# Kernel optimization log

Hardware: AMD Instinct MI355X
Metric: run time of the kernel (lower is better)

The kernel has to match this reference:

```python
import jax, jax.numpy as jnp
import numpy as np

SEQ, BATCH, D, N = 256, 4, 512, 32768
TEMP = 0.5


def setup_inputs() -> dict:
    key = jax.random.key(0)
    ks = jax.random.split(key, 16)
    d = D
    # xavier_uniform with gain 1/sqrt(2) for square [d,d]: limit = gain*sqrt(6/(d+d))
    lim_t = (1.0 / np.sqrt(2.0)) * np.sqrt(6.0 / (d + d))
    lim_g1 = np.sqrt(6.0 / (2 * d + d))  # default kaiming-ish scale approximated by xavier
    lim_g2 = np.sqrt(6.0 / (d + 1))
    inp = {
        "q": jax.random.normal(ks[0], (SEQ, BATCH, D), dtype=jnp.float32),
        "prev_layer_output": jax.random.normal(ks[1], (SEQ, BATCH, D), dtype=jnp.float32),
        "Wq": jax.random.uniform(ks[2], (D, D), jnp.float32, -lim_t, lim_t),
        "bq": jnp.zeros((D,), jnp.float32),
        "Wk": jax.random.uniform(ks[3], (D, D), jnp.float32, -lim_t, lim_t),
        "bk": jnp.zeros((D,), jnp.float32),
        "Wv": jax.random.uniform(ks[4], (D, D), jnp.float32, -lim_t, lim_t),
        "bv": jnp.zeros((D,), jnp.float32),
        "Wg1": jax.random.uniform(ks[5], (D, 2 * D), jnp.float32, -lim_g1, lim_g1),
        "bg1": jnp.zeros((D,), jnp.float32),
        "Wg2": jax.random.uniform(ks[6], (1, D), jnp.float32, -lim_g2, lim_g2),
        "bg2": jnp.zeros((1,), jnp.float32),
        "dstore_k": jax.random.normal(ks[7], (N, D), dtype=jnp.float32),
        "dstore_v": jax.random.normal(ks[8], (N, D), dtype=jnp.float32),
    }
    return inp


def reference(q, prev_layer_output, Wq, bq, Wk, bk, Wv, bv, Wg1, bg1, Wg2, bg2, dstore_k, dstore_v):
    # [S,B,D] -> [B,S,D]
    qb = jnp.transpose(q, (1, 0, 2))
    prevb = jnp.transpose(prev_layer_output, (1, 0, 2))
    # enable_tune projections
    _q = qb @ Wq.T + bq                      # [B,S,D]
    _k = dstore_k @ Wk.T + bk                # [N,D]
    _v = dstore_v @ Wv.T + bv                # [N,D]
    _q = _q * (D ** -0.5)
    # attention over datastore, temperature-scaled softmax
    logits = jnp.einsum("bsd,nd->bsn", _q, _k) / TEMP  # [B,S,N]
    w = jax.nn.softmax(logits, axis=-1)
    attn = jnp.einsum("bsn,nd->bsd", w, _v)            # [B,S,D]
    # gated residual fusion
    cat = jnp.concatenate([attn, prevb], axis=-1)      # [B,S,2D]
    h = jax.nn.relu(cat @ Wg1.T + bg1)                 # [B,S,D]
    sigma = jax.nn.sigmoid(h @ Wg2.T + bg2)            # [B,S,1]
    res = attn * sigma + prevb * (1.0 - sigma)
    return jnp.transpose(res, (1, 0, 2))               # [S,B,D]
```

## Files before the change

kernel.cpp:

```cpp
#include <hip/hip_runtime.h>
#include <hip/hip_bf16.h>
#include <cstdint>
#include <cstddef>


typedef unsigned short u16;
typedef u16    u16x8 __attribute__((ext_vector_type(8)));
typedef u16    u16x4 __attribute__((ext_vector_type(4)));
typedef __bf16 bf16x8 __attribute__((ext_vector_type(8)));
typedef float  f32x4 __attribute__((ext_vector_type(4)));

#define MFMA16(a, b, c) __builtin_amdgcn_mfma_f32_16x16x32_bf16( \
    __builtin_bit_cast(bf16x8, (a)), __builtin_bit_cast(bf16x8, (b)), (c), 0, 0, 0)

__device__ __forceinline__ u16 f2bf(float f) {
  unsigned u = __builtin_bit_cast(unsigned, f);
  u += 0x7fffu + ((u >> 16) & 1u);
  return (u16)(u >> 16);
}

__global__ __launch_bounds__(256) void prep_cvt(const float* __restrict__ src,
                                                u16* __restrict__ dst) {
  size_t i = ((size_t)blockIdx.x * 256 + threadIdx.x) * 4;
  float4 v = *(const float4*)(src + i);
  u16x4 o = {f2bf(v.x), f2bf(v.y), f2bf(v.z), f2bf(v.w)};
  *(u16x4*)(dst + i) = o;
}

__global__ __launch_bounds__(256) void prep_vt(const float* __restrict__ v,
                                               u16* __restrict__ vt) {
  __shared__ u16 Lt[64 * 72];
  const int n0 = blockIdx.x * 64, d0 = blockIdx.y * 64;
  const int t = threadIdx.x;
  const int n = t >> 2, c4 = t & 3;
#pragma unroll
  for (int i = 0; i < 4; i++) {
    int col = (c4 + 4 * i) * 4;
    float4 x = *(const float4*)(v + (size_t)(n0 + n) * 512 + d0 + col);
    Lt[(col + 0) * 72 + n] = f2bf(x.x);
    Lt[(col + 1) * 72 + n] = f2bf(x.y);
    Lt[(col + 2) * 72 + n] = f2bf(x.z);
    Lt[(col + 3) * 72 + n] = f2bf(x.w);
  }
  __syncthreads();
#pragma unroll
  for (int u = 0; u < 2; u++) {
    int unit = t + 256 * u;
    int d = unit >> 3, un = unit & 7;
    *(u16x8*)(vt + (size_t)(d0 + d) * 32768 + n0 + un * 8) =
        *(const u16x8*)&Lt[d * 72 + un * 8];
  }
}

template <bool TRANSB, bool CONCAT, bool RELU, bool OUTBF16, bool ROWSCALE>
__global__ __launch_bounds__(256, 2) void gemm64(
    const float* __restrict__ A, const float* __restrict__ A2,
    const float* __restrict__ B, const float* __restrict__ bias,
    const float* __restrict__ lvec, float alpha, void* __restrict__ Cv,
    int M, int N, int K) {
  __shared__ u16 As[64 * 72];
  __shared__ u16 Bs[64 * 72];
  const int tid = threadIdx.x;
  const int w = tid >> 6, lane = tid & 63, quad = lane >> 4, l15 = lane & 15;
  const int m0 = blockIdx.y * 64, n0 = blockIdx.x * 64;
  const int arow = tid >> 2, ac4 = tid & 3;
  float rs = 1.0f;
  if (ROWSCALE) rs = 1.0f / lvec[m0 + arow];
  const f32x4 fzero = {0.f, 0.f, 0.f, 0.f};
  f32x4 acc[4];
#pragma unroll
  for (int i = 0; i < 4; i++) acc[i] = fzero;

  for (int k0 = 0; k0 < K; k0 += 64) {
    __syncthreads();
    {
      const float* src;
      if (CONCAT)
        src = (k0 < 512) ? (A + (size_t)(m0 + arow) * 512 + k0)
                         : (A2 + (size_t)(m0 + arow) * 512 + (k0 - 512));
      else
        src = A + (size_t)(m0 + arow) * K + k0;
#pragma unroll
      for (int i = 0; i < 4; i++) {
        int col = (ac4 + 4 * i) * 4;
        float4 x = *(const float4*)(src + col);
        if (ROWSCALE) { x.x *= rs; x.y *= rs; x.z *= rs; x.w *= rs; }
        u16x4 o = {f2bf(x.x), f2bf(x.y), f2bf(x.z), f2bf(x.w)};
        *(u16x4*)&As[arow * 72 + col] = o;
      }
    }
    if (TRANSB) {
      const float* src = B + (size_t)(n0 + arow) * K + k0;
#pragma unroll
      for (int i = 0; i < 4; i++) {
        int col = (ac4 + 4 * i) * 4;
        float4 x = *(const float4*)(src + col);
        u16x4 o = {f2bf(x.x), f2bf(x.y), f2bf(x.z), f2bf(x.w)};
        *(u16x4*)&Bs[arow * 72 + col] = o;
      }
    } else {
      const float* src = B + (size_t)(k0 + arow) * N + n0;
#pragma unroll
      for (int i = 0; i < 4; i++) {
        int col = (ac4 + 4 * i) * 4;
        float4 x = *(const float4*)(src + col);
        Bs[(col + 0) * 72 + arow] = f2bf(x.x);
        Bs[(col + 1) * 72 + arow] = f2bf(x.y);
        Bs[(col + 2) * 72 + arow] = f2bf(x.z);
        Bs[(col + 3) * 72 + arow] = f2bf(x.w);
      }
    }
    __syncthreads();
#pragma unroll
    for (int ks = 0; ks < 2; ks++) {
      u16x8 af = *(const u16x8*)&As[(w * 16 + l15) * 72 + ks * 32 + quad * 8];
#pragma unroll
      for (int nt = 0; nt < 4; nt++) {
        u16x8 bf = *(const u16x8*)&Bs[(nt * 16 + l15) * 72 + ks * 32 + quad * 8];
        acc[nt] = MFMA16(af, bf, acc[nt]);
      }
    }
  }
#pragma unroll
  for (int nt = 0; nt < 4; nt++) {
    int col = n0 + nt * 16 + l15;
    float b = bias ? bias[col] : 0.f;
#pragma unroll
    for (int i = 0; i < 4; i++) {
      int row = m0 + w * 16 + quad * 4 + i;
      float y = (acc[nt][i] + b) * alpha;
      if (RELU) y = fmaxf(y, 0.f);
      if (OUTBF16)
        ((u16*)Cv)[(size_t)row * N + col] = f2bf(y);
      else
        ((float*)Cv)[(size_t)row * N + col] = y;
    }
  }
}

__global__ void cq_kernel(const float* __restrict__ q1,
                          const float* __restrict__ bk,
                          float* __restrict__ cq) {
  int r = blockIdx.x, lane = threadIdx.x;
  float s = 0.f;
#pragma unroll
  for (int k = 0; k < 512; k += 64) s += q1[(size_t)r * 512 + k + lane] * bk[k + lane];
#pragma unroll
  for (int off = 32; off; off >>= 1) s += __shfl_down(s, off, 64);
  if (lane == 0) cq[r] = 2.0f * s;
}

__global__ __launch_bounds__(512, 2) void flash(
    const u16* __restrict__ kbf,
    const u16* __restrict__ vt,
    const u16* __restrict__ q2,
    const float* __restrict__ cq,
    float* __restrict__ racc,
    float* __restrict__ lacc) {
  __shared__ u16 Ks[32 * 520];
  __shared__ u16 Es[64 * 40];
  const int tid = threadIdx.x;
  const int w = tid >> 6, lane = tid & 63, quad = lane >> 4, l15 = lane & 15;
  const int qt = blockIdx.x & 15, ch = blockIdx.x >> 4;
  const int qbase = qt * 64;
  const int qg = w >> 1, nh = w & 1;
  const int colb = w * 64;

  u16x8 qf[16];
  {
    const u16* qp = q2 + (size_t)(qbase + qg * 16 + l15) * 512 + quad * 8;
#pragma unroll
    for (int ks = 0; ks < 16; ks++) qf[ks] = *(const u16x8*)(qp + ks * 32);
  }
  float cq4[4];
#pragma unroll
  for (int i = 0; i < 4; i++) cq4[i] = cq[qbase + qg * 16 + quad * 4 + i];
  float lp[4] = {0.f, 0.f, 0.f, 0.f};
  const f32x4 fzero = {0.f, 0.f, 0.f, 0.f};
  f32x4 acc[4][4];
#pragma unroll
  for (int a = 0; a < 4; a++)
#pragma unroll
    for (int b = 0; b < 4; b++) acc[a][b] = fzero;

  u16x8 st[4];
  u16x8 bvp[4];
  int n0 = ch * 2048;
#pragma unroll
  for (int u = 0; u < 4; u++) {
    int flat = tid + u * 512;
    st[u] = *(const u16x8*)(kbf + (size_t)(n0 + (flat >> 6)) * 512 + (flat & 63) * 8);
  }
#pragma unroll
  for (int ct = 0; ct < 4; ct++)
    bvp[ct] = *(const u16x8*)(vt + (size_t)(colb + ct * 16 + l15) * 32768 + n0 + quad * 8);

#pragma unroll 1
  for (int sub = 0; sub < 64; ++sub) {
    n0 = ch * 2048 + sub * 32;
    __syncthreads();
#pragma unroll
    for (int u = 0; u < 4; u++) {
      int flat = tid + u * 512;
      *(u16x8*)&Ks[(flat >> 6) * 520 + (flat & 63) * 8] = st[u];
    }
    if (sub + 1 < 64) {
      int n1 = n0 + 32;
#pragma unroll
      for (int u = 0; u < 4; u++) {
        int flat = tid + u * 512;
        st[u] = *(const u16x8*)(kbf + (size_t)(n1 + (flat >> 6)) * 512 + (flat & 63) * 8);
      }
    }
    __syncthreads();
    f32x4 s = fzero;
#pragma unroll
    for (int ks = 0; ks < 16; ks++) {
      u16x8 bfg = *(const u16x8*)&Ks[(nh * 16 + l15) * 520 + ks * 32 + quad * 8];
      s = MFMA16(qf[ks], bfg, s);
    }
#pragma unroll
    for (int i = 0; i < 4; i++) {
      float e = __expf(s[i] + cq4[i]);
      lp[i] += e;
      Es[(qg * 16 + quad * 4 + i) * 40 + nh * 16 + l15] = f2bf(e);
    }
    __syncthreads();
    u16x8 ef[4];
#pragma unroll
    for (int q2i = 0; q2i < 4; q2i++)
      ef[q2i] = *(const u16x8*)&Es[(q2i * 16 + l15) * 40 + quad * 8];
#pragma unroll
    for (int ct = 0; ct < 4; ct++) {
#pragma unroll
      for (int q2i = 0; q2i < 4; q2i++)
        acc[q2i][ct] = MFMA16(ef[q2i], bvp[ct], acc[q2i][ct]);
    }
    if (sub + 1 < 64) {
      int n1 = n0 + 32;
#pragma unroll
      for (int ct = 0; ct < 4; ct++)
        bvp[ct] = *(const u16x8*)(vt + (size_t)(colb + ct * 16 + l15) * 32768 + n1 + quad * 8);
    }
  }
#pragma unroll
  for (int q2i = 0; q2i < 4; q2i++)
#pragma unroll
    for (int ct = 0; ct < 4; ct++) {
      int col = colb + ct * 16 + l15;
#pragma unroll
      for (int i = 0; i < 4; i++) {
        int row = qbase + q2i * 16 + quad * 4 + i;
        atomicAdd(&racc[(size_t)row * 512 + col], acc[q2i][ct][i]);
      }
    }
#pragma unroll
  for (int i = 0; i < 4; i++) {
    float v = lp[i];
#pragma unroll
    for (int off = 1; off < 16; off <<= 1) v += __shfl_xor(v, off, 64);
    if (l15 == 0) atomicAdd(&lacc[qbase + qg * 16 + quad * 4 + i], v);
  }
}

__global__ __launch_bounds__(256) void finalize(
    const float* __restrict__ h, const float* __restrict__ attn,
    const float* __restrict__ prev, const float* __restrict__ wg2,
    const float* __restrict__ bg2, float* __restrict__ out) {
  __shared__ float red[4];
  int r = blockIdx.x, t = threadIdx.x;
  const float* hr = h + (size_t)r * 512;
  float p = hr[t] * wg2[t] + hr[t + 256] * wg2[t + 256];
#pragma unroll
  for (int off = 32; off; off >>= 1) p += __shfl_down(p, off, 64);
  if ((t & 63) == 0) red[t >> 6] = p;
  __syncthreads();
  float dot = red[0] + red[1] + red[2] + red[3];
  float sg = 1.f / (1.f + __expf(-(dot + bg2[0])));
  size_t base = (size_t)r * 512;
  out[base + t] = attn[base + t] * sg + prev[base + t] * (1.f - sg);
  out[base + t + 256] = attn[base + t + 256] * sg + prev[base + t + 256] * (1.f - sg);
}

extern "C" void kernel_launch(void* const* d_in, const int* in_sizes, int n_in,
                              void* d_out, int out_size, void* d_ws, size_t ws_size,
                              hipStream_t stream) {
  const float* q    = (const float*)d_in[0];
  const float* prev = (const float*)d_in[1];
  const float* Wq   = (const float*)d_in[2];
  const float* bq   = (const float*)d_in[3];
  const float* Wk   = (const float*)d_in[4];
  const float* bk   = (const float*)d_in[5];
  const float* Wv   = (const float*)d_in[6];
  const float* bv   = (const float*)d_in[7];
  const float* Wg1  = (const float*)d_in[8];
  const float* bg1  = (const float*)d_in[9];
  const float* Wg2  = (const float*)d_in[10];
  const float* bg2  = (const float*)d_in[11];
  const float* dk   = (const float*)d_in[12];
  const float* dv   = (const float*)d_in[13];
  float* out = (float*)d_out;

  char* ws = (char*)d_ws;
  u16*   kbf  = (u16*)(ws);
  u16*   vt   = (u16*)(ws + 33554432);
  float* racc = (float*)(ws + 67108864);
  float* lacc = (float*)(ws + 69206016);
  float* cqv  = (float*)(ws + 69210112);
  u16*   q2   = (u16*)(ws + 69214208);
  float* q1   = (float*)(ws + 70262784);
  float* attn = (float*)(ws + 72359936);
  float* h    = q1;

  prep_cvt<<<16384, 256, 0, stream>>>(dk, kbf);
  prep_vt<<<dim3(512, 8), 256, 0, stream>>>(dv, vt);
  gemm64<true, false, false, false, false><<<dim3(8, 16), 256, 0, stream>>>(
      q, nullptr, Wq, bq, nullptr, 0.044194173824159216f, q1, 1024, 512, 512);
  cq_kernel<<<1024, 64, 0, stream>>>(q1, bk, cqv);
  gemm64<false, false, false, true, false><<<dim3(8, 16), 256, 0, stream>>>(
      q1, nullptr, Wk, nullptr, nullptr, 2.0f, q2, 1024, 512, 512);
  hipMemsetAsync(racc, 0, 2097152 + 4096, stream);
  flash<<<256, 512, 0, stream>>>(kbf, vt, q2, cqv, racc, lacc);
  gemm64<true, false, false, false, true><<<dim3(8, 16), 256, 0, stream>>>(
      racc, nullptr, Wv, bv, lacc, 1.0f, attn, 1024, 512, 512);
  gemm64<true, true, true, false, false><<<dim3(8, 16), 256, 0, stream>>>(
      attn, prev, Wg1, bg1, nullptr, 1.0f, h, 1024, 512, 1024);
  finalize<<<1024, 256, 0, stream>>>(h, attn, prev, Wg2, bg2, out);
}
```

Before: 417.4 us.

## Software-pipeline flash loop with double-buffered exp tile and remapped block order

Restructures the datastore attention loop into a two-stage software pipeline. The QK logits of the current chunk overlap the PV accumulation of the previous chunk, using a double-buffered exp tile in shared memory, which removes one barrier per chunk. It also adds s_setprio around the MFMA sections and remaps blockIdx so neighbouring blocks share datastore chunks differently, which may improve L2 locality. The cost is extra register pressure from two V fragment sets and a more complex prologue and epilogue.

```diff
diff --git a/kernel.cpp b/kernel.cpp
--- a/kernel.cpp
+++ b/kernel.cpp
@@ -158,13 +158,15 @@
     float* __restrict__ racc,
     float* __restrict__ lacc) {
   __shared__ u16 Ks[32 * 520];
-  __shared__ u16 Es[64 * 40];
+  __shared__ u16 Es[2][64 * 40];
   const int tid = threadIdx.x;
   const int w = tid >> 6, lane = tid & 63, quad = lane >> 4, l15 = lane & 15;
-  const int qt = blockIdx.x & 15, ch = blockIdx.x >> 4;
+  const int x = blockIdx.x & 7, j = blockIdx.x >> 3;
+  const int ch = 2 * x + (j & 1), qt = j >> 1;
   const int qbase = qt * 64;
   const int qg = w >> 1, nh = w & 1;
   const int colb = w * 64;
+  const int nbase = ch * 2048;
 
   u16x8 qf[16];
   {
@@ -184,65 +186,116 @@
     for (int b = 0; b < 4; b++) acc[a][b] = fzero;
 
   u16x8 st[4];
-  u16x8 bvp[4];
-  int n0 = ch * 2048;
-#pragma unroll
-  for (int u = 0; u < 4; u++) {
-    int flat = tid + u * 512;
-    st[u] = *(const u16x8*)(kbf + (size_t)(n0 + (flat >> 6)) * 512 + (flat & 63) * 8);
-  }
-#pragma unroll
-  for (int ct = 0; ct < 4; ct++)
-    bvp[ct] = *(const u16x8*)(vt + (size_t)(colb + ct * 16 + l15) * 32768 + n0 + quad * 8);
+  u16x8 bvA[4], bvB[4];
+
+#define STORE_KS()                                                      \
+  {                                                                     \
+    _Pragma("unroll") for (int u = 0; u < 4; u++) {                     \
+      int flat = tid + u * 512;                                         \
+      *(u16x8*)&Ks[(flat >> 6) * 520 + (flat & 63) * 8] = st[u];        \
+    }                                                                   \
+  }
+#define LOAD_K(SUBN)                                                    \
+  {                                                                     \
+    _Pragma("unroll") for (int u = 0; u < 4; u++) {                     \
+      int flat = tid + u * 512;                                         \
+      st[u] = *(const u16x8*)(kbf +                                     \
+          (size_t)(nbase + (SUBN) * 32 + (flat >> 6)) * 512 +           \
+          (flat & 63) * 8);                                             \
+    }                                                                   \
+  }
+#define LOAD_V(BV, SUBN)                                                \
+  {                                                                     \
+    _Pragma("unroll") for (int ct = 0; ct < 4; ct++)                    \
+      BV[ct] = *(const u16x8*)(vt +                                     \
+          (size_t)(colb + ct * 16 + l15) * 32768 +                      \
+          nbase + (SUBN) * 32 + quad * 8);                              \
+  }
+#define LOGITS(SV)                                                      \
+  {                                                                     \
+    _Pragma("unroll") for (int ks = 0; ks < 16; ks++) {                 \
+      u16x8 bfg = *(const u16x8*)&Ks[(nh * 16 + l15) * 520 + ks * 32 +  \
+                                     quad * 8];                         \
+      SV = MFMA16(qf[ks], bfg, SV);                                     \
+    }                                                                   \
+  }
+#define PV_STEP(ER, BV)                                                 \
+  {                                                                     \
+    u16x8 ef[4];                                                        \
+    _Pragma("unroll") for (int q2i = 0; q2i < 4; q2i++)                 \
+      ef[q2i] = *(const u16x8*)&(ER)[(q2i * 16 + l15) * 40 + quad * 8]; \
+    _Pragma("unroll") for (int ct = 0; ct < 4; ct++)                    \
+      _Pragma("unroll") for (int q2i = 0; q2i < 4; q2i++)               \
+        acc[q2i][ct] = MFMA16(ef[q2i], BV[ct], acc[q2i][ct]);           \
+  }
+#define EXPW(EW, SV)                                                    \
+  {                                                                     \
+    _Pragma("unroll") for (int i = 0; i < 4; i++) {                     \
+      float e = __expf(SV[i] + cq4[i]);                                 \
+      lp[i] += e;                                                       \
+      (EW)[(qg * 16 + quad * 4 + i) * 40 + nh * 16 + l15] = f2bf(e);    \
+    }                                                                   \
+  }
+
+  LOAD_K(0);
+  STORE_KS();
+  __syncthreads();
+  LOAD_K(1);
+  LOAD_V(bvA, 0);
+  {
+    f32x4 s = fzero;
+    LOGITS(s);
+    EXPW(Es[0], s);
+  }
 
 #pragma unroll 1
-  for (int sub = 0; sub < 64; ++sub) {
-    n0 = ch * 2048 + sub * 32;
-    __syncthreads();
-#pragma unroll
-    for (int u = 0; u < 4; u++) {
-      int flat = tid + u * 512;
-      *(u16x8*)&Ks[(flat >> 6) * 520 + (flat & 63) * 8] = st[u];
-    }
-    if (sub + 1 < 64) {
-      int n1 = n0 + 32;
-#pragma unroll
-      for (int u = 0; u < 4; u++) {
-        int flat = tid + u * 512;
-        st[u] = *(const u16x8*)(kbf + (size_t)(n1 + (flat >> 6)) * 512 + (flat & 63) * 8);
-      }
-    }
-    __syncthreads();
+  for (int sb = 1; sb < 63; sb += 2) {
+    __syncthreads();
+    STORE_KS();
+    __syncthreads();
+    LOAD_K(sb + 1);
+    LOAD_V(bvB, sb);
+    __builtin_amdgcn_s_setprio(1);
     f32x4 s = fzero;
-#pragma unroll
-    for (int ks = 0; ks < 16; ks++) {
-      u16x8 bfg = *(const u16x8*)&Ks[(nh * 16 + l15) * 520 + ks * 32 + quad * 8];
-      s = MFMA16(qf[ks], bfg, s);
-    }
-#pragma unroll
-    for (int i = 0; i < 4; i++) {
-      float e = __expf(s[i] + cq4[i]);
-      lp[i] += e;
-      Es[(qg * 16 + quad * 4 + i) * 40 + nh * 16 + l15] = f2bf(e);
-    }
-    __syncthreads();
-    u16x8 ef[4];
-#pragma unroll
-    for (int q2i = 0; q2i < 4; q2i++)
-      ef[q2i] = *(const u16x8*)&Es[(q2i * 16 + l15) * 40 + quad * 8];
-#pragma unroll
-    for (int ct = 0; ct < 4; ct++) {
-#pragma unroll
-      for (int q2i = 0; q2i < 4; q2i++)
-        acc[q2i][ct] = MFMA16(ef[q2i], bvp[ct], acc[q2i][ct]);
-    }
-    if (sub + 1 < 64) {
-      int n1 = n0 + 32;
-#pragma unroll
-      for (int ct = 0; ct < 4; ct++)
-        bvp[ct] = *(const u16x8*)(vt + (size_t)(colb + ct * 16 + l15) * 32768 + n1 + quad * 8);
-    }
-  }
+    LOGITS(s);
+    PV_STEP(Es[0], bvA);
+    __builtin_amdgcn_s_setprio(0);
+    EXPW(Es[1], s);
+    __syncthreads();
+    STORE_KS();
+    __syncthreads();
+    LOAD_K(sb + 2);
+    LOAD_V(bvA, sb + 1);
+    __builtin_amdgcn_s_setprio(1);
+    f32x4 t = fzero;
+    LOGITS(t);
+    PV_STEP(Es[1], bvB);
+    __builtin_amdgcn_s_setprio(0);
+    EXPW(Es[0], t);
+  }
+
+  __syncthreads();
+  STORE_KS();
+  __syncthreads();
+  LOAD_V(bvB, 63);
+  {
+    __builtin_amdgcn_s_setprio(1);
+    f32x4 s = fzero;
+    LOGITS(s);
+    PV_STEP(Es[0], bvA);
+    __builtin_amdgcn_s_setprio(0);
+    EXPW(Es[1], s);
+  }
+  __syncthreads();
+  PV_STEP(Es[1], bvB);
+
+#undef STORE_KS
+#undef LOAD_K
+#undef LOAD_V
+#undef LOGITS
+#undef PV_STEP
+#undef EXPW
+
 #pragma unroll
   for (int q2i = 0; q2i < 4; q2i++)
 #pragma unroll
```

After: 403.5 us. 3.3% less time.

## Pre-swizzle K into MFMA fragment layout and pipeline flash loop with double-buffered E

Applied to the files above, without the earlier changes.

The K conversion kernel now writes bf16 K in per-lane MFMA fragment order, so the flash kernel loads its K operands directly from global memory into registers instead of staging them through LDS. The flash loop is software-pipelined: the P·V step for the previous sub-tile overlaps with the logits of the current one, using a double-buffered exp tile and one barrier per iteration instead of three. It also splits the logits accumulation into two chains, raises wave priority around the P·V MFMAs, and remaps block indices to change L2 locality. The cost is more register pressure (16 K fragments per lane) and redundant global K loads across waves that share the same K rows.

```diff
diff --git a/kernel.cpp b/kernel.cpp
--- a/kernel.cpp
+++ b/kernel.cpp
@@ -19,12 +19,24 @@
   return (u16)(u >> 16);
 }
 
-__global__ __launch_bounds__(256) void prep_cvt(const float* __restrict__ src,
-                                                u16* __restrict__ dst) {
-  size_t i = ((size_t)blockIdx.x * 256 + threadIdx.x) * 4;
-  float4 v = *(const float4*)(src + i);
-  u16x4 o = {f2bf(v.x), f2bf(v.y), f2bf(v.z), f2bf(v.w)};
-  *(u16x4*)(dst + i) = o;
+__global__ __launch_bounds__(256) void prep_kfrag(const float* __restrict__ src,
+                                                  u16* __restrict__ dst) {
+  const int sub = blockIdx.x;
+  const int t = threadIdx.x;
+  const float* s0 = src + (size_t)sub * 32 * 512;
+  u16* d0 = dst + (size_t)sub * 16384;
+#pragma unroll
+  for (int u = 0; u < 8; u++) {
+    int ci = t + 256 * u;
+    int nh = ci >> 10, ks = (ci >> 6) & 15, ln = ci & 63;
+    int qd = ln >> 4, l15 = ln & 15;
+    const float* sp = s0 + (size_t)(nh * 16 + l15) * 512 + ks * 32 + qd * 8;
+    float4 a = *(const float4*)sp;
+    float4 b = *(const float4*)(sp + 4);
+    u16x8 o = {f2bf(a.x), f2bf(a.y), f2bf(a.z), f2bf(a.w),
+               f2bf(b.x), f2bf(b.y), f2bf(b.z), f2bf(b.w)};
+    *(u16x8*)(d0 + (size_t)ci * 8) = o;
+  }
 }
 
 __global__ __launch_bounds__(256) void prep_vt(const float* __restrict__ v,
@@ -151,17 +163,17 @@
 }
 
 __global__ __launch_bounds__(512, 2) void flash(
-    const u16* __restrict__ kbf,
+    const u16* __restrict__ kfr,
     const u16* __restrict__ vt,
     const u16* __restrict__ q2,
     const float* __restrict__ cq,
     float* __restrict__ racc,
     float* __restrict__ lacc) {
-  __shared__ u16 Ks[32 * 520];
-  __shared__ u16 Es[64 * 40];
+  __shared__ u16 Es[2][64 * 40];
   const int tid = threadIdx.x;
   const int w = tid >> 6, lane = tid & 63, quad = lane >> 4, l15 = lane & 15;
-  const int qt = blockIdx.x & 15, ch = blockIdx.x >> 4;
+  const int x = blockIdx.x & 7, j = blockIdx.x >> 3;
+  const int ch = 2 * x + (j & 1), qt = j >> 1;
   const int qbase = qt * 64;
   const int qg = w >> 1, nh = w & 1;
   const int colb = w * 64;
@@ -183,66 +195,88 @@
 #pragma unroll
     for (int b = 0; b < 4; b++) acc[a][b] = fzero;
 
-  u16x8 st[4];
-  u16x8 bvp[4];
-  int n0 = ch * 2048;
-#pragma unroll
-  for (int u = 0; u < 4; u++) {
-    int flat = tid + u * 512;
-    st[u] = *(const u16x8*)(kbf + (size_t)(n0 + (flat >> 6)) * 512 + (flat & 63) * 8);
-  }
-#pragma unroll
-  for (int ct = 0; ct < 4; ct++)
-    bvp[ct] = *(const u16x8*)(vt + (size_t)(colb + ct * 16 + l15) * 32768 + n0 + quad * 8);
+  const u16* kp0 = kfr + (((size_t)(ch * 64) * 2 + nh) * 16) * 512 + lane * 8;
+  const u16* vp0 = vt + (size_t)(colb + l15) * 32768 + ch * 2048 + quad * 8;
+
+  u16x8 kf[16];
+  u16x8 bv[4];
+
+#define LOAD_KF(SUB)                                                     \
+  {                                                                      \
+    const u16* kps = kp0 + (size_t)(SUB) * 16384;                        \
+    _Pragma("unroll") for (int ks = 0; ks < 16; ks++)                    \
+        kf[ks] = *(const u16x8*)(kps + ks * 512);                        \
+  }
+#define LOAD_V(SUB)                                                      \
+  {                                                                      \
+    _Pragma("unroll") for (int ct = 0; ct < 4; ct++)                     \
+        bv[ct] = *(const u16x8*)(vp0 + (size_t)ct * (16 * 32768) +       \
+                                 (SUB) * 32);                            \
+  }
+#define LOGITS(SV)                                                       \
+  {                                                                      \
+    f32x4 s0_ = fzero, s1_ = fzero;                                      \
+    _Pragma("unroll") for (int ks = 0; ks < 16; ks += 2) {               \
+      s0_ = MFMA16(qf[ks], kf[ks], s0_);                                 \
+      s1_ = MFMA16(qf[ks + 1], kf[ks + 1], s1_);                         \
+    }                                                                    \
+    SV = s0_ + s1_;                                                      \
+  }
+#define PV_STEP(ER)                                                      \
+  {                                                                      \
+    u16x8 ef[4];                                                         \
+    _Pragma("unroll") for (int q2i = 0; q2i < 4; q2i++)                  \
+      ef[q2i] = *(const u16x8*)&(ER)[(q2i * 16 + l15) * 40 + quad * 8];  \
+    _Pragma("unroll") for (int ct = 0; ct < 4; ct++)                     \
+      _Pragma("unroll") for (int q2i = 0; q2i < 4; q2i++)                \
+        acc[q2i][ct] = MFMA16(ef[q2i], bv[ct], acc[q2i][ct]);            \
+  }
+#define EXPW(EW, SV)                                                     \
+  {                                                                      \
+    _Pragma("unroll") for (int i = 0; i < 4; i++) {                      \
+      float e = __expf(SV[i] + cq4[i]);                                  \
+      lp[i] += e;                                                        \
+      (EW)[(qg * 16 + quad * 4 + i) * 40 + nh * 16 + l15] = f2bf(e);     \
+    }                                                                    \
+  }
+#define BARRIER()                                                        \
+  {                                                                      \
+    asm volatile("s_waitcnt lgkmcnt(0)" ::: "memory");                   \
+    __builtin_amdgcn_s_barrier();                                        \
+    __builtin_amdgcn_sched_barrier(0);                                   \
+  }
+
+  LOAD_KF(0);
+  LOAD_V(0);
+  {
+    f32x4 s;
+    LOGITS(s);
+    EXPW(Es[0], s);
+  }
 
 #pragma unroll 1
-  for (int sub = 0; sub < 64; ++sub) {
-    n0 = ch * 2048 + sub * 32;
-    __syncthreads();
-#pragma unroll
-    for (int u = 0; u < 4; u++) {
-      int flat = tid + u * 512;
-      *(u16x8*)&Ks[(flat >> 6) * 520 + (flat & 63) * 8] = st[u];
-    }
-    if (sub + 1 < 64) {
-      int n1 = n0 + 32;
-#pragma unroll
-      for (int u = 0; u < 4; u++) {
-        int flat = tid + u * 512;
-        st[u] = *(const u16x8*)(kbf + (size_t)(n1 + (flat >> 6)) * 512 + (flat & 63) * 8);
-      }
-    }
-    __syncthreads();
-    f32x4 s = fzero;
-#pragma unroll
-    for (int ks = 0; ks < 16; ks++) {
-      u16x8 bfg = *(const u16x8*)&Ks[(nh * 16 + l15) * 520 + ks * 32 + quad * 8];
-      s = MFMA16(qf[ks], bfg, s);
-    }
-#pragma unroll
-    for (int i = 0; i < 4; i++) {
-      float e = __expf(s[i] + cq4[i]);
-      lp[i] += e;
-      Es[(qg * 16 + quad * 4 + i) * 40 + nh * 16 + l15] = f2bf(e);
-    }
-    __syncthreads();
-    u16x8 ef[4];
-#pragma unroll
-    for (int q2i = 0; q2i < 4; q2i++)
-      ef[q2i] = *(const u16x8*)&Es[(q2i * 16 + l15) * 40 + quad * 8];
-#pragma unroll
-    for (int ct = 0; ct < 4; ct++) {
-#pragma unroll
-      for (int q2i = 0; q2i < 4; q2i++)
-        acc[q2i][ct] = MFMA16(ef[q2i], bvp[ct], acc[q2i][ct]);
-    }
-    if (sub + 1 < 64) {
-      int n1 = n0 + 32;
-#pragma unroll
-      for (int ct = 0; ct < 4; ct++)
-        bvp[ct] = *(const u16x8*)(vt + (size_t)(colb + ct * 16 + l15) * 32768 + n1 + quad * 8);
-    }
-  }
+  for (int sub = 1; sub < 64; ++sub) {
+    BARRIER();
+    LOAD_KF(sub);
+    __builtin_amdgcn_s_setprio(1);
+    PV_STEP(Es[(sub - 1) & 1]);
+    __builtin_amdgcn_s_setprio(0);
+    LOAD_V(sub);
+    f32x4 s;
+    LOGITS(s);
+    EXPW(Es[sub & 1], s);
+  }
+
+  BARRIER();
+  PV_STEP(Es[1]);
+
+#undef LOAD_KF
+#undef LOAD_V
+#undef LOGITS
+#undef PV_STEP
+#undef EXPW
+#undef BARRIER
+
 #pragma unroll
   for (int q2i = 0; q2i < 4; q2i++)
 #pragma unroll
@@ -302,7 +336,7 @@
   float* out = (float*)d_out;
 
   char* ws = (char*)d_ws;
-  u16*   kbf  = (u16*)(ws);
+  u16*   kfr  = (u16*)(ws);
   u16*   vt   = (u16*)(ws + 33554432);
   float* racc = (float*)(ws + 67108864);
   float* lacc = (float*)(ws + 69206016);
@@ -312,7 +346,7 @@
   float* attn = (float*)(ws + 72359936);
   float* h    = q1;
 
-  prep_cvt<<<16384, 256, 0, stream>>>(dk, kbf);
+  prep_kfrag<<<1024, 256, 0, stream>>>(dk, kfr);
   prep_vt<<<dim3(512, 8), 256, 0, stream>>>(dv, vt);
   gemm64<true, false, false, false, false><<<dim3(8, 16), 256, 0, stream>>>(
       q, nullptr, Wq, bq, nullptr, 0.044194173824159216f, q1, 1024, 512, 512);
@@ -320,7 +354,7 @@
   gemm64<false, false, false, true, false><<<dim3(8, 16), 256, 0, stream>>>(
       q1, nullptr, Wk, nullptr, nullptr, 2.0f, q2, 1024, 512, 512);
   hipMemsetAsync(racc, 0, 2097152 + 4096, stream);
-  flash<<<256, 512, 0, stream>>>(kbf, vt, q2, cqv, racc, lacc);
+  flash<<<256, 512, 0, stream>>>(kfr, vt, q2, cqv, racc, lacc);
   gemm64<true, false, false, false, true><<<dim3(8, 16), 256, 0, stream>>>(
       racc, nullptr, Wv, bv, lacc, 1.0f, attn, 1024, 512, 512);
   gemm64<true, true, true, false, false><<<dim3(8, 16), 256, 0, stream>>>(
```

Measured after the change: 431.3 us. 3.3% more time.
